# Performance work log

Hardware: AMD Instinct MI355X
Metric: run time of the kernel (lower is better)

Reference implementation:

```python
import jax, jax.numpy as jnp
import numpy as np


def conv(x, w, b=None, stride=1, pad=0):
    out = jax.lax.conv_general_dilated(x, w, (stride, stride), [(pad, pad), (pad, pad)],
                                       dimension_numbers=('NCHW', 'OIHW', 'NCHW'))
    if b is not None:
        out = out + b[None, :, None, None]
    return out


def fsm(x, att_w, conv_w):
    # FeatureSelectionModule: global-avg-pool -> 1x1 conv -> sigmoid gate, residual, 1x1 proj
    gap = jnp.mean(x, axis=(2, 3), keepdims=True)
    atten = jax.nn.sigmoid(conv(gap, att_w))
    return conv(x + x * atten, conv_w)


def mdcn(x, offset, mask, weight, bias, pad=1, G=8):
    # Modulated deformable conv v2: stride 1, dilation 1, conv groups 1, G deformable groups.
    N, C, H, W = x.shape
    Co, Ci, kh, kw = weight.shape
    K = kh * kw
    Cg = C // G
    off = offset.reshape(N, G, 2, K, H, W)          # per-group (y, x) offsets per kernel tap
    msk = mask.reshape(N, G, 1, K, H, W)
    ky, kx = jnp.meshgrid(jnp.arange(kh), jnp.arange(kw), indexing='ij')
    py = (jnp.arange(H, dtype=x.dtype)[None, None, None, :, None] - pad) + ky.reshape(1, 1, K, 1, 1) + off[:, :, 0]
    px = (jnp.arange(W, dtype=x.dtype)[None, None, None, None, :] - pad) + kx.reshape(1, 1, K, 1, 1) + off[:, :, 1]
    y0 = jnp.floor(py)
    x0 = jnp.floor(px)
    wy1 = py - y0
    wy0 = 1.0 - wy1
    wx1 = px - x0
    wx0 = 1.0 - wx1
    xg = x.reshape(N, G, Cg, H * W)

    def gather(iy, ix):
        valid = (iy >= 0) & (iy <= H - 1) & (ix >= 0) & (ix <= W - 1)
        idx = (jnp.clip(iy, 0, H - 1) * W + jnp.clip(ix, 0, W - 1)).astype(jnp.int32)
        v = jnp.take_along_axis(xg, idx.reshape(N, G, 1, K * H * W), axis=3)
        return v.reshape(N, G, Cg, K, H, W) * valid[:, :, None].astype(x.dtype)

    val = ((wy0 * wx0)[:, :, None] * gather(y0, x0)
         + (wy0 * wx1)[:, :, None] * gather(y0, x0 + 1)
         + (wy1 * wx0)[:, :, None] * gather(y0 + 1, x0)
         + (wy1 * wx1)[:, :, None] * gather(y0 + 1, x0 + 1))
    val = val * msk                                   # [N,G,Cg,K,H,W]
    out = jnp.einsum('ngckhw,ogck->nohw', val, weight.reshape(Co, G, Cg, K))
    return out + bias[None, :, None, None]


def align(feat_l, feat_s, att_w, fsm_w, off_w, om_w, om_b, dcn_w, dcn_b):
    # FeatureAlign_V2
    N, Cs, H, W = feat_s.shape[0], feat_s.shape[1], feat_l.shape[2], feat_l.shape[3]
    feat_up = jax.image.resize(feat_s, (N, Cs, H, W), 'bilinear')  # align_corners=False
    feat_arm = fsm(feat_l, att_w, fsm_w)
    off_feat = conv(jnp.concatenate([feat_arm, feat_up * 2.0], axis=1), off_w)
    om = conv(off_feat, om_w, om_b, pad=1)            # conv_offset_mask: 3*G*K channels
    o1, o2, mk = jnp.split(om, 3, axis=1)
    offset = jnp.concatenate([o1, o2], axis=1)
    mask = jax.nn.sigmoid(mk)
    feat_align = jax.nn.relu(mdcn(feat_up, offset, mask, dcn_w, dcn_b))
    return feat_align + feat_arm


def setup_inputs() -> dict:
    key = jax.random.key(0)
    ks = iter(jax.random.split(key, 64))

    def w(shape):
        fan_in = shape[1] * shape[2] * shape[3]
        return jax.random.normal(next(ks), shape, jnp.float32) / np.float32(np.sqrt(fan_in))

    def b(n):
        return jnp.zeros((n,), jnp.float32)

    d = {}
    d['c2'] = jax.random.normal(next(ks), (1, 256, 128, 128), jnp.float32)
    d['c3'] = jax.random.normal(next(ks), (1, 512, 64, 64), jnp.float32)
    d['c4'] = jax.random.normal(next(ks), (1, 1024, 32, 32), jnp.float32)
    d['c5'] = jax.random.normal(next(ks), (1, 2048, 16, 16), jnp.float32)
    OC = 256
    OM = 8 * 3 * 9  # deformable_groups * (2 offsets + 1 mask) * k*k = 216
    for tag, in_nc in (('16', 1024), ('8', 512), ('4', 256)):
        d['att_w' + tag] = w((in_nc, in_nc, 1, 1))
        d['fsm_w' + tag] = w((OC, in_nc, 1, 1))
        d['off_w' + tag] = w((OC, 2 * OC, 1, 1))
        d['om_w' + tag] = w((OM, OC, 3, 3))
        d['om_b' + tag] = b(OM)
        d['dcn_w' + tag] = w((OC, OC, 3, 3))
        d['dcn_b' + tag] = b(OC)
        d['out_w' + tag] = w((OC, OC, 3, 3))
        d['out_b' + tag] = b(OC)
    d['lat_w'] = w((OC, 2048, 1, 1))
    d['lat_b'] = b(OC)
    return d


def reference(c2, c3, c4, c5,
              att_w16, fsm_w16, off_w16, om_w16, om_b16, dcn_w16, dcn_b16, out_w16, out_b16,
              att_w8, fsm_w8, off_w8, om_w8, om_b8, dcn_w8, dcn_b8, out_w8, out_b8,
              att_w4, fsm_w4, off_w4, om_w4, om_b4, dcn_w4, dcn_b4, out_w4, out_b4,
              lat_w, lat_b):
    # top-down pass, coarsest first (matches FAN.forward with reversed inputs)
    p5 = conv(c5, lat_w, lat_b)
    f16 = align(c4, p5, att_w16, fsm_w16, off_w16, om_w16, om_b16, dcn_w16, dcn_b16)
    p4 = conv(f16, out_w16, out_b16, pad=1)
    f8 = align(c3, f16, att_w8, fsm_w8, off_w8, om_w8, om_b8, dcn_w8, dcn_b8)
    p3 = conv(f8, out_w8, out_b8, pad=1)
    f4 = align(c2, f8, att_w4, fsm_w4, off_w4, om_w4, om_b4, dcn_w4, dcn_b4)
    p2 = conv(f4, out_w4, out_b4, pad=1)
    return (p2, p3, p4, p5)
```

## Files before the change

kernel.cpp:

```cpp
#include <hip/hip_runtime.h>
#include <hip/hip_bf16.h>

typedef __hip_bfloat16 bf16;
typedef __attribute__((ext_vector_type(8))) short bf16x8;
typedef __attribute__((ext_vector_type(4))) float floatx4;

__device__ __forceinline__ float b2f(bf16 v) { return __bfloat162float(v); }
__device__ __forceinline__ bf16 f2b(float v) { return __float2bfloat16(v); }
__device__ __forceinline__ float us2f(unsigned short u) {
  union { unsigned int i; float f; } v; v.i = ((unsigned int)u) << 16; return v.f;
}
__device__ __forceinline__ unsigned short f2us(float f) {
  bf16 h = f2b(f); return *(unsigned short*)&h;
}

__global__ __launch_bounds__(256) void gap_kernel(const float* __restrict__ x,
                                                  float* __restrict__ gap,
                                                  int HW, float inv) {
  int c = blockIdx.x;
  const float* p = x + (size_t)c * HW;
  float s = 0.f;
  for (int i = threadIdx.x; i < HW; i += 256) s += p[i];
  __shared__ float red[256];
  red[threadIdx.x] = s;
  __syncthreads();
  for (int w = 128; w > 0; w >>= 1) {
    if (threadIdx.x < w) red[threadIdx.x] += red[threadIdx.x + w];
    __syncthreads();
  }
  if (threadIdx.x == 0) gap[c] = red[0] * inv;
}

__global__ __launch_bounds__(256) void atten_kernel(const float* __restrict__ w,
                                                    const float* __restrict__ gap,
                                                    float* __restrict__ scale, int Ci) {
  int wave = threadIdx.x >> 6, lane = threadIdx.x & 63;
  int o = blockIdx.x * 4 + wave;
  const float4* wr = (const float4*)(w + (size_t)o * Ci);
  const float4* g4 = (const float4*)gap;
  int n4 = Ci >> 2;
  float s = 0.f;
  for (int i = lane; i < n4; i += 64) {
    float4 a = wr[i], b = g4[i];
    s += a.x * b.x + a.y * b.y + a.z * b.z + a.w * b.w;
  }
#pragma unroll
  for (int off = 32; off > 0; off >>= 1) s += __shfl_down(s, off);
  if (lane == 0) scale[o] = 1.f + 1.f / (1.f + expf(-s));
}

__global__ __launch_bounds__(256) void upsample2x_nhwc_kernel(
    const bf16* __restrict__ src, bf16* __restrict__ dst, int Hs, int Ws) {
  int p = blockIdx.x;
  int c = threadIdx.x;
  int W = Ws * 2;
  int y = p / W, x = p - y * W;
  float fy = y * 0.5f - 0.25f;
  float fx = x * 0.5f - 0.25f;
  int y0 = (int)floorf(fy), x0 = (int)floorf(fx);
  float wy1 = fy - (float)y0, wx1 = fx - (float)x0;
  int y0c = min(max(y0, 0), Hs - 1);
  int y1c = min(max(y0 + 1, 0), Hs - 1);
  int x0c = min(max(x0, 0), Ws - 1);
  int x1c = min(max(x0 + 1, 0), Ws - 1);
  float v00 = b2f(src[(size_t)(y0c * Ws + x0c) * 256 + c]);
  float v01 = b2f(src[(size_t)(y0c * Ws + x1c) * 256 + c]);
  float v10 = b2f(src[(size_t)(y1c * Ws + x0c) * 256 + c]);
  float v11 = b2f(src[(size_t)(y1c * Ws + x1c) * 256 + c]);
  float v = (1.f - wy1) * ((1.f - wx1) * v00 + wx1 * v01)
          + wy1 * ((1.f - wx1) * v10 + wx1 * v11);
  dst[(size_t)p * 256 + c] = f2b(v);
}

__global__ __launch_bounds__(256) void packw1_kernel(const float* __restrict__ w,
                                                     bf16* __restrict__ BP, int K) {
  int idx = blockIdx.x * 256 + threadIdx.x;
  int j = idx & 7;
  int o = (idx >> 3) & 255;
  int kc8 = idx >> 11;
  int k = kc8 * 8 + j;
  BP[idx] = f2b(w[(size_t)o * K + k]);
}

__global__ __launch_bounds__(256) void packwd_kernel(const float* __restrict__ w,
                                                     bf16* __restrict__ BP) {
  int idx = blockIdx.x * 256 + threadIdx.x;
  int j = idx & 7;
  int o = (idx >> 3) & 255;
  int k8 = idx >> 11;
  int k = k8 * 8 + j;
  int tap = k >> 8;
  int ci = k & 255;
  BP[idx] = f2b(w[((size_t)o * 256 + ci) * 9 + tap]);
}

__global__ __launch_bounds__(256) void packw3_kernel(const float* __restrict__ w,
                                                     bf16* __restrict__ BP,
                                                     int Ci, int Co) {
  int idx = blockIdx.x * 256 + threadIdx.x;
  int total = Ci * 9 * 256;
  if (idx >= total) return;
  int j = idx & 7;
  int t1 = idx >> 3;
  int o = t1 & 255;
  int t2 = t1 >> 8;
  int q = t2 & 3;
  int t3 = t2 >> 2;
  int tap = t3 % 9;
  int c = t3 / 9;
  int ci = c * 32 + q * 8 + j;
  float v = (o < Co) ? w[((size_t)o * Ci + ci) * 9 + tap] : 0.f;
  BP[idx] = f2b(v);
}

template <bool NCHW1, typename TA1>
__global__ __launch_bounds__(256) void conv1x1_mfma_kernel(
    const TA1* __restrict__ A1, const float* __restrict__ scaleA,
    const bf16* __restrict__ A2, float scaleB,
    int Ci1, int Ci2, int HW,
    const bf16* __restrict__ BP, const float* __restrict__ bias,
    float* __restrict__ out1, bf16* __restrict__ out2, int ns2) {
  __shared__ __align__(16) bf16 sA[1024];
  int p0 = blockIdx.x * 32;
  int tid = threadIdx.x;
  int pix = tid & 31, sub = tid >> 5;
  int pix2 = tid >> 3, sub8 = tid & 7;
  int lane = tid & 63, wave = tid >> 6;
  int pg = wave & 1, cg = wave >> 1;
  int q = lane >> 4, n = lane & 15;

  floatx4 acc[4];
#pragma unroll
  for (int nt = 0; nt < 4; ++nt) acc[nt] = (floatx4)0.f;

  int nch = (Ci1 + Ci2) >> 5;
  for (int kc = 0; kc < nch; ++kc) {
    int ci0 = kc << 5;
    if (NCHW1 && ci0 < Ci1) {
#pragma unroll
      for (int it = 0; it < 4; ++it) {
        int cil = it * 8 + sub;
        float x = (float)A1[(size_t)(ci0 + cil) * HW + p0 + pix];
        if (scaleA) x *= scaleA[ci0 + cil];
        sA[((cil >> 3) * 32 + pix) * 8 + (cil & 7)] = f2b(x);
      }
    } else {
      const bf16* src; int cb; bool scl;
      if (!NCHW1 && ci0 < Ci1) {
        src = (const bf16*)(const void*)A1; cb = ci0; scl = false;
      } else {
        src = A2; cb = ci0 - Ci1; scl = true;
      }
      ushort4 raw = *(const ushort4*)&src[(size_t)(p0 + pix2) * 256 + cb + sub8 * 4];
      if (scl) {
        raw.x = f2us(us2f(raw.x) * scaleB);
        raw.y = f2us(us2f(raw.y) * scaleB);
        raw.z = f2us(us2f(raw.z) * scaleB);
        raw.w = f2us(us2f(raw.w) * scaleB);
      }
      *(ushort4*)&sA[((sub8 >> 1) * 32 + pix2) * 8 + (sub8 & 1) * 4] = raw;
    }
    __syncthreads();
    bf16x8 a = *(const bf16x8*)&sA[(q * 32 + pg * 16 + n) * 8];
    const bf16* bp = BP + ((size_t)(kc * 4 + q) * 256 + blockIdx.y * 128 + cg * 64) * 8;
#pragma unroll
    for (int nt = 0; nt < 4; ++nt) {
      bf16x8 b = *(const bf16x8*)&bp[(nt * 16 + n) * 8];
      acc[nt] = __builtin_amdgcn_mfma_f32_16x16x32_bf16(a, b, acc[nt], 0, 0, 0);
    }
    __syncthreads();
  }

  int pbase = p0 + pg * 16 + q * 4;
#pragma unroll
  for (int nt = 0; nt < 4; ++nt) {
    int o = blockIdx.y * 128 + cg * 64 + nt * 16 + n;
    float bv = bias ? bias[o] : 0.f;
#pragma unroll
    for (int r = 0; r < 4; ++r) {
      float v = acc[nt][r] + bv;
      if (out1) out1[(size_t)o * HW + pbase + r] = v;
      if (out2) out2[(size_t)(pbase + r) * ns2 + o] = f2b(v);
    }
  }
}

__global__ __launch_bounds__(256) void conv1x1_part_kernel(
    const float* __restrict__ A1, int HW,
    const bf16* __restrict__ BP, float* __restrict__ PART) {
  __shared__ __align__(16) bf16 sA[1024];
  int p0 = blockIdx.x * 32;
  int tid = threadIdx.x;
  int pix = tid & 31, sub = tid >> 5;
  int lane = tid & 63, wave = tid >> 6;
  int pg = wave & 1, cg = wave >> 1;
  int q = lane >> 4, n = lane & 15;

  floatx4 acc[4];
#pragma unroll
  for (int nt = 0; nt < 4; ++nt) acc[nt] = (floatx4)0.f;

  int kc0 = blockIdx.z * 8;
  for (int kcl = 0; kcl < 8; ++kcl) {
    int kc = kc0 + kcl;
    int ci0 = kc << 5;
#pragma unroll
    for (int it = 0; it < 4; ++it) {
      int cil = it * 8 + sub;
      sA[((cil >> 3) * 32 + pix) * 8 + (cil & 7)] =
          f2b(A1[(size_t)(ci0 + cil) * HW + p0 + pix]);
    }
    __syncthreads();
    bf16x8 a = *(const bf16x8*)&sA[(q * 32 + pg * 16 + n) * 8];
    const bf16* bp = BP + ((size_t)(kc * 4 + q) * 256 + blockIdx.y * 128 + cg * 64) * 8;
#pragma unroll
    for (int nt = 0; nt < 4; ++nt) {
      bf16x8 b = *(const bf16x8*)&bp[(nt * 16 + n) * 8];
      acc[nt] = __builtin_amdgcn_mfma_f32_16x16x32_bf16(a, b, acc[nt], 0, 0, 0);
    }
    __syncthreads();
  }

  int pbase = p0 + pg * 16 + q * 4;
#pragma unroll
  for (int nt = 0; nt < 4; ++nt) {
    int o = blockIdx.y * 128 + cg * 64 + nt * 16 + n;
#pragma unroll
    for (int r = 0; r < 4; ++r)
      PART[((size_t)blockIdx.z * 256 + o) * HW + pbase + r] = acc[nt][r];
  }
}

__global__ __launch_bounds__(256) void reduce_p5_kernel(
    const float* __restrict__ PART, const float* __restrict__ bias,
    float* __restrict__ out1, bf16* __restrict__ out2, int HW, int KS) {
  int o = blockIdx.x;
  int p = threadIdx.x;
  float s = bias[o];
  for (int z = 0; z < KS; ++z) s += PART[((size_t)z * 256 + o) * HW + p];
  out1[(size_t)o * HW + p] = s;
  out2[(size_t)p * 256 + o] = f2b(s);
}

template <int S>
__global__ __launch_bounds__(256) void conv3x3v2_kernel(
    const bf16* __restrict__ in, const bf16* __restrict__ BP,
    const float* __restrict__ bias,
    int H, int W, int Co,
    float* __restrict__ out1, bf16* __restrict__ out2, int ns2) {
  constexpr int P = 32 * S + 2;
  constexpr int TASKS = 3 * P * 8;
  constexpr int ITS = (TASKS + 255) / 256;
  __shared__ __align__(16) bf16 sA[2][4 * 3 * P * 8];
  int HW = H * W;
  int segs = W / (32 * S);
  int y = blockIdx.x / segs;
  int x0 = (blockIdx.x - y * segs) * (32 * S);
  int tid = threadIdx.x;
  int lane = tid & 63, wave = tid >> 6;
  int pg = wave & 1, cg = wave >> 1;
  int q = lane >> 4, n = lane & 15;

  int dstIdx[ITS], srcOff[ITS];
  bool act[ITS], val[ITS];
#pragma unroll
  for (int it = 0; it < ITS; ++it) {
    int tt = it * 256 + tid;
    act[it] = (tt < TASKS);
    int sub8 = tt & 7;
    int rp = tt >> 3;
    int row = rp / P;
    int pxl = rp - row * P;
    int yy = y + row - 1;
    int xg = x0 + pxl - 1;
    bool v = act[it] && ((unsigned)yy < (unsigned)H) && ((unsigned)xg < (unsigned)W);
    val[it] = v;
    srcOff[it] = v ? ((yy * W + xg) * 256 + sub8 * 4) : 0;
    dstIdx[it] = (((sub8 >> 1) * 3 + row) * P + pxl) * 8 + (sub8 & 1) * 4;
  }

  ushort4 pv[ITS];
  auto load_regs = [&](int kc) {
    int cb = kc << 5;
#pragma unroll
    for (int it = 0; it < ITS; ++it) {
      ushort4 z = {0, 0, 0, 0};
      pv[it] = val[it] ? *(const ushort4*)&in[(size_t)srcOff[it] + cb] : z;
    }
  };
  auto store_lds = [&](int buf) {
#pragma unroll
    for (int it = 0; it < ITS; ++it)
      if (act[it]) *(ushort4*)&sA[buf][dstIdx[it]] = pv[it];
  };

  floatx4 acc[S][4];
#pragma unroll
  for (int s = 0; s < S; ++s)
#pragma unroll
    for (int nt = 0; nt < 4; ++nt) acc[s][nt] = (floatx4)0.f;

  load_regs(0);
  store_lds(0);
  __syncthreads();
  load_regs(1);

  for (int kc = 0; kc < 8; ++kc) {
    const bf16* sv = &sA[kc & 1][0];
    const bf16* bpc = BP + (size_t)kc * 73728;
#pragma unroll
    for (int tap = 0; tap < 9; ++tap) {
      int ty = tap / 3, tx = tap % 3;
      bf16x8 a[S];
#pragma unroll
      for (int s = 0; s < S; ++s)
        a[s] = *(const bf16x8*)&sv[((q * 3 + ty) * P + tx + s * 32 + pg * 16 + n) * 8];
      const bf16* bp = bpc + ((size_t)(tap * 4 + q) * 256 + blockIdx.y * 128 + cg * 64) * 8;
#pragma unroll
      for (int nt = 0; nt < 4; ++nt) {
        bf16x8 b = *(const bf16x8*)&bp[(nt * 16 + n) * 8];
#pragma unroll
        for (int s = 0; s < S; ++s)
          acc[s][nt] = __builtin_amdgcn_mfma_f32_16x16x32_bf16(a[s], b, acc[s][nt], 0, 0, 0);
      }
    }
    if (kc < 7) {
      store_lds((kc + 1) & 1);
      __syncthreads();
      if (kc < 6) load_regs(kc + 2);
    }
  }

#pragma unroll
  for (int s = 0; s < S; ++s) {
    int pbase = y * W + x0 + s * 32 + pg * 16 + q * 4;
#pragma unroll
    for (int nt = 0; nt < 4; ++nt) {
      int o = blockIdx.y * 128 + cg * 64 + nt * 16 + n;
      if (o < Co) {
        float bv = bias ? bias[o] : 0.f;
#pragma unroll
        for (int r = 0; r < 4; ++r) {
          float v = acc[s][nt][r] + bv;
          if (out1) out1[(size_t)o * HW + pbase + r] = v;
          if (out2) out2[(size_t)(pbase + r) * ns2 + o] = f2b(v);
        }
      }
    }
  }
}

__global__ __launch_bounds__(512, 4) void mdcn_mfma_kernel(
    const bf16* __restrict__ UPn, const bf16* __restrict__ OM,
    const bf16* __restrict__ BP, const float* __restrict__ dcn_b,
    const bf16* __restrict__ ARM, bf16* __restrict__ F,
    int H, int W, int wshift) {
  __shared__ __align__(16) bf16 sval[2][32 * 272];
  __shared__ float4 mw[2304];
  __shared__ int mi[2304];
  int pb = blockIdx.x * 32;
  int tid = threadIdx.x;

  for (int t2 = tid; t2 < 2304; t2 += 512) {
    int px_ = t2 & 31, g = (t2 >> 5) & 7, tap = t2 >> 8;
    int ky = tap / 3, kx = tap - ky * 3;
    int p = pb + px_;
    int y = p >> wshift, x = p & (W - 1);
    const bf16* omp = OM + (size_t)p * 216;
    float dy = b2f(omp[g * 18 + tap]);
    float dx = b2f(omp[g * 18 + 9 + tap]);
    float mm = 1.f / (1.f + expf(-b2f(omp[144 + g * 9 + tap])));
    float fpy = (float)(y - 1 + ky) + dy;
    float fpx = (float)(x - 1 + kx) + dx;
    fpy = fminf(fmaxf(fpy, -1.0e4f), 1.0e4f);
    fpx = fminf(fmaxf(fpx, -1.0e4f), 1.0e4f);
    float fy0 = floorf(fpy), fx0 = floorf(fpx);
    float wy1 = fpy - fy0, wx1 = fpx - fx0;
    float wy0 = 1.f - wy1, wx0 = 1.f - wx1;
    int iy0 = (int)fy0, ix0 = (int)fx0;
    bool vy0 = (unsigned)iy0 < (unsigned)H;
    bool vy1 = (unsigned)(iy0 + 1) < (unsigned)H;
    bool vx0 = (unsigned)ix0 < (unsigned)W;
    bool vx1 = (unsigned)(ix0 + 1) < (unsigned)W;
    float w00 = (vy0 && vx0) ? mm * wy0 * wx0 : 0.f;
    float w01 = (vy0 && vx1) ? mm * wy0 * wx1 : 0.f;
    float w10 = (vy1 && vx0) ? mm * wy1 * wx0 : 0.f;
    float w11 = (vy1 && vx1) ? mm * wy1 * wx1 : 0.f;
    int iy0c = min(max(iy0, 0), H - 1);
    int iy1c = min(max(iy0 + 1, 0), H - 1);
    int ix0c = min(max(ix0, 0), W - 1);
    int ix1c = min(max(ix0 + 1, 0), W - 1);
    mw[t2] = make_float4(w00, w01, w10, w11);
    mi[t2] = (iy0c * W + ix0c) | ((ix1c - ix0c) << 20) | ((iy1c - iy0c) << 21);
  }
  __syncthreads();

  int l4 = tid & 7;
  int px = (tid >> 3) & 31;
  int gh = tid >> 8;
  int lane = tid & 63, wave = tid >> 6;
  int q = lane >> 4, n = lane & 15;
  int rowb = l4 >> 1;
  int woff = px * 8 + (l4 & 1) * 4;

  floatx4 acc[2][2];
#pragma unroll
  for (int m = 0; m < 2; ++m)
#pragma unroll
    for (int nt = 0; nt < 2; ++nt) acc[m][nt] = (floatx4)0.f;

  auto gather = [&](int t) {
    bf16* sv = &sval[t & 1][0];
    int base = t * 256 + px + gh * 128;
#pragma unroll
    for (int gg = 0; gg < 4; ++gg) {
      int g = gh * 4 + gg;
      float4 wv = mw[base + gg * 32];
      int mv = mi[base + gg * 32];
      int idx = mv & 0x3FFFF;
      int dxs = (mv >> 20) & 1;
      int dyW = ((mv >> 21) & 1) * W;
      const bf16* up = UPn + (size_t)idx * 256 + g * 32 + l4 * 4;
      ushort4 u00 = *(const ushort4*)(up);
      ushort4 u01 = *(const ushort4*)(up + dxs * 256);
      ushort4 u10 = *(const ushort4*)(up + dyW * 256);
      ushort4 u11 = *(const ushort4*)(up + (dyW + dxs) * 256);
      ushort4 o4;
      o4.x = f2us(wv.x * us2f(u00.x) + wv.y * us2f(u01.x)
                + wv.z * us2f(u10.x) + wv.w * us2f(u11.x));
      o4.y = f2us(wv.x * us2f(u00.y) + wv.y * us2f(u01.y)
                + wv.z * us2f(u10.y) + wv.w * us2f(u11.y));
      o4.z = f2us(wv.x * us2f(u00.z) + wv.y * us2f(u01.z)
                + wv.z * us2f(u10.z) + wv.w * us2f(u11.z));
      o4.w = f2us(wv.x * us2f(u00.w) + wv.y * us2f(u01.w)
                + wv.z * us2f(u10.w) + wv.w * us2f(u11.w));
      *(ushort4*)&sv[(g * 4 + rowb) * 272 + woff] = o4;
    }
  };

  gather(0);
  for (int t = 0; t < 9; ++t) {
    __syncthreads();
    if (t < 8) gather(t + 1);
    const bf16* sv = &sval[t & 1][0];
    const bf16* bpt = BP + ((size_t)(t * 32) * 256 + wave * 32) * 8;
#pragma unroll
    for (int kc = 0; kc < 8; ++kc) {
      int R = kc * 4 + q;
      bf16x8 a0 = *(const bf16x8*)&sv[R * 272 + n * 8];
      bf16x8 a1 = *(const bf16x8*)&sv[R * 272 + (16 + n) * 8];
      const bf16* bp = bpt + (size_t)R * 2048;
      bf16x8 b0 = *(const bf16x8*)&bp[n * 8];
      bf16x8 b1 = *(const bf16x8*)&bp[(16 + n) * 8];
      acc[0][0] = __builtin_amdgcn_mfma_f32_16x16x32_bf16(a0, b0, acc[0][0], 0, 0, 0);
      acc[0][1] = __builtin_amdgcn_mfma_f32_16x16x32_bf16(a0, b1, acc[0][1], 0, 0, 0);
      acc[1][0] = __builtin_amdgcn_mfma_f32_16x16x32_bf16(a1, b0, acc[1][0], 0, 0, 0);
      acc[1][1] = __builtin_amdgcn_mfma_f32_16x16x32_bf16(a1, b1, acc[1][1], 0, 0, 0);
    }
  }

#pragma unroll
  for (int m = 0; m < 2; ++m) {
#pragma unroll
    for (int nt = 0; nt < 2; ++nt) {
      int o = wave * 32 + nt * 16 + n;
      float bv = dcn_b[o];
#pragma unroll
      for (int r = 0; r < 4; ++r) {
        int p = pb + m * 16 + q * 4 + r;
        float v = fmaxf(acc[m][nt][r] + bv, 0.f) + b2f(ARM[(size_t)p * 256 + o]);
        F[(size_t)p * 256 + o] = f2b(v);
      }
    }
  }
}

extern "C" void kernel_launch(void* const* d_in, const int* in_sizes, int n_in,
                              void* d_out, int out_size, void* d_ws, size_t ws_size,
                              hipStream_t stream) {
  const float* c2 = (const float*)d_in[0];
  const float* c3 = (const float*)d_in[1];
  const float* c4 = (const float*)d_in[2];
  const float* c5 = (const float*)d_in[3];
  const float* lat_w = (const float*)d_in[31];
  const float* lat_b = (const float*)d_in[32];
  float* out = (float*)d_out;
  (void)ws_size; (void)in_sizes; (void)n_in; (void)out_size;

  const size_t p2_off = 0;
  const size_t p3_off = 4194304;
  const size_t p4_off = p3_off + 1048576;
  const size_t p5_off = p4_off + 262144;

  char* ws = (char*)d_ws;
  bf16* UPn = (bf16*)(ws);
  bf16* ARM = (bf16*)(ws + 8388608);
  bf16* FB  = (bf16*)(ws + 16777216);
  bf16* P5N = (bf16*)(ws + 25165824);
  bf16* BPB = (bf16*)(ws + 25296896);
  float* GAP = (float*)(ws + 26476544);
  float* SC  = (float*)(ws + 26484736);
  bf16* OM = (bf16*)(out + p2_off);
  float* PART = (float*)ws;

  packw1_kernel<<<2048, 256, 0, stream>>>(lat_w, BPB, 2048);
  conv1x1_part_kernel<<<dim3(8, 2, 8), 256, 0, stream>>>(c5, 256, BPB, PART);
  reduce_p5_kernel<<<256, 256, 0, stream>>>(PART, lat_b, out + p5_off, P5N, 256, 8);

  struct Lv {
    const float* featl; int Ci; int H; int W; int wshift;
    float* pdst; int wbase;
  };
  Lv levels[3] = {
      {c4, 1024, 32, 32, 5, out + p4_off, 4},
      {c3, 512, 64, 64, 6, out + p3_off, 13},
      {c2, 256, 128, 128, 7, out + p2_off, 22},
  };

  for (int li = 0; li < 3; ++li) {
    const Lv& L = levels[li];
    const float* att_w = (const float*)d_in[L.wbase + 0];
    const float* fsm_w = (const float*)d_in[L.wbase + 1];
    const float* off_w = (const float*)d_in[L.wbase + 2];
    const float* om_w  = (const float*)d_in[L.wbase + 3];
    const float* om_b  = (const float*)d_in[L.wbase + 4];
    const float* dcn_w = (const float*)d_in[L.wbase + 5];
    const float* dcn_b = (const float*)d_in[L.wbase + 6];
    const float* out_w = (const float*)d_in[L.wbase + 7];
    const float* out_b = (const float*)d_in[L.wbase + 8];
    int HW = L.H * L.W;

    upsample2x_nhwc_kernel<<<HW, 256, 0, stream>>>(
        (li == 0) ? P5N : FB, UPn, L.H / 2, L.W / 2);
    gap_kernel<<<L.Ci, 256, 0, stream>>>(L.featl, GAP, HW, 1.f / (float)HW);
    atten_kernel<<<L.Ci / 4, 256, 0, stream>>>(att_w, GAP, SC, L.Ci);
    packw1_kernel<<<L.Ci, 256, 0, stream>>>(fsm_w, BPB, L.Ci);
    conv1x1_mfma_kernel<true, float><<<dim3(HW / 32, 2), 256, 0, stream>>>(
        L.featl, SC, nullptr, 0.f, L.Ci, 0, HW, BPB, nullptr,
        nullptr, ARM, 256);
    packw1_kernel<<<512, 256, 0, stream>>>(off_w, BPB, 512);
    conv1x1_mfma_kernel<false, bf16><<<dim3(HW / 32, 2), 256, 0, stream>>>(
        ARM, nullptr, UPn, 2.f, 256, 256, HW, BPB, nullptr,
        nullptr, FB, 256);
    packw3_kernel<<<2304, 256, 0, stream>>>(om_w, BPB, 256, 216);
    if (li == 2)
      conv3x3v2_kernel<2><<<dim3(HW / 64, 2), 256, 0, stream>>>(
          FB, BPB, om_b, L.H, L.W, 216, nullptr, OM, 216);
    else
      conv3x3v2_kernel<1><<<dim3(HW / 32, 2), 256, 0, stream>>>(
          FB, BPB, om_b, L.H, L.W, 216, nullptr, OM, 216);
    packwd_kernel<<<2304, 256, 0, stream>>>(dcn_w, BPB);
    mdcn_mfma_kernel<<<HW / 32, 512, 0, stream>>>(
        UPn, OM, BPB, dcn_b, ARM, FB, L.H, L.W, L.wshift);
    packw3_kernel<<<2304, 256, 0, stream>>>(out_w, BPB, 256, 256);
    if (li == 2)
      conv3x3v2_kernel<2><<<dim3(HW / 64, 2), 256, 0, stream>>>(
          FB, BPB, out_b, L.H, L.W, 256, L.pdst, nullptr, 256);
    else
      conv3x3v2_kernel<1><<<dim3(HW / 32, 2), 256, 0, stream>>>(
          FB, BPB, out_b, L.H, L.W, 256, L.pdst, nullptr, 256);
  }
}
```

Before: 723.7 us.

## Fuse per-level weight packing into one launch and overlap MDCN gathers with MFMA

Per level, the five separate weight-packing launches are merged into one pack_level_kernel that writes into distinct buffers, so per-launch overhead drops and packs no longer serialize between convolutions. Some packed buffers are placed in unused parts of the output region. In the deformable conv kernel, the gather is split into a global-load phase issued before the MFMA loop and a blend/store phase after it, so memory latency hides behind matrix math. This costs 64 extra ushort registers per thread, which may lower occupancy, and relies on output scratch space not being overwritten before use.

```diff
diff --git a/kernel.cpp b/kernel.cpp
--- a/kernel.cpp
+++ b/kernel.cpp
@@ -82,24 +82,40 @@
   BP[idx] = f2b(w[(size_t)o * K + k]);
 }
 
-__global__ __launch_bounds__(256) void packwd_kernel(const float* __restrict__ w,
-                                                     bf16* __restrict__ BP) {
-  int idx = blockIdx.x * 256 + threadIdx.x;
-  int j = idx & 7;
-  int o = (idx >> 3) & 255;
-  int k8 = idx >> 11;
-  int k = k8 * 8 + j;
-  int tap = k >> 8;
-  int ci = k & 255;
-  BP[idx] = f2b(w[((size_t)o * 256 + ci) * 9 + tap]);
-}
-
-__global__ __launch_bounds__(256) void packw3_kernel(const float* __restrict__ w,
-                                                     bf16* __restrict__ BP,
-                                                     int Ci, int Co) {
-  int idx = blockIdx.x * 256 + threadIdx.x;
-  int total = Ci * 9 * 256;
-  if (idx >= total) return;
+__global__ __launch_bounds__(256) void pack_level_kernel(
+    const float* __restrict__ fsm_w, int Ci,
+    const float* __restrict__ off_w, const float* __restrict__ om_w,
+    const float* __restrict__ dcn_w, const float* __restrict__ out_w,
+    bf16* __restrict__ BPfsm, bf16* __restrict__ BPoff, bf16* __restrict__ BPom,
+    bf16* __restrict__ BPdcn, bf16* __restrict__ BPout) {
+  int b = blockIdx.x;
+  if (b < Ci) {
+    int idx = b * 256 + threadIdx.x;
+    int j = idx & 7, o = (idx >> 3) & 255, k = (idx >> 11) * 8 + j;
+    BPfsm[idx] = f2b(fsm_w[(size_t)o * Ci + k]);
+    return;
+  }
+  b -= Ci;
+  if (b < 512) {
+    int idx = b * 256 + threadIdx.x;
+    int j = idx & 7, o = (idx >> 3) & 255, k = (idx >> 11) * 8 + j;
+    BPoff[idx] = f2b(off_w[(size_t)o * 512 + k]);
+    return;
+  }
+  b -= 512;
+  const float* w;
+  bf16* BP;
+  int Co;
+  if (b < 2304) { w = om_w; BP = BPom; Co = 216; }
+  else if (b < 4608) {
+    int idx = (b - 2304) * 256 + threadIdx.x;
+    int j = idx & 7, o = (idx >> 3) & 255;
+    int k = (idx >> 11) * 8 + j;
+    int tap = k >> 8, ci = k & 255;
+    BPdcn[idx] = f2b(dcn_w[((size_t)o * 256 + ci) * 9 + tap]);
+    return;
+  } else { w = out_w; BP = BPout; Co = 256; b -= 2304; }
+  int idx = (b % 2304) * 256 + threadIdx.x;
   int j = idx & 7;
   int t1 = idx >> 3;
   int o = t1 & 255;
@@ -109,7 +125,7 @@
   int tap = t3 % 9;
   int c = t3 / 9;
   int ci = c * 32 + q * 8 + j;
-  float v = (o < Co) ? w[((size_t)o * Ci + ci) * 9 + tap] : 0.f;
+  float v = (o < Co) ? w[((size_t)o * 256 + ci) * 9 + tap] : 0.f;
   BP[idx] = f2b(v);
 }
 
@@ -409,22 +425,31 @@
 #pragma unroll
     for (int nt = 0; nt < 2; ++nt) acc[m][nt] = (floatx4)0.f;
 
-  auto gather = [&](int t) {
-    bf16* sv = &sval[t & 1][0];
+  ushort4 gl[4][4];
+  auto gatherLoad = [&](int t) {
     int base = t * 256 + px + gh * 128;
 #pragma unroll
     for (int gg = 0; gg < 4; ++gg) {
       int g = gh * 4 + gg;
-      float4 wv = mw[base + gg * 32];
       int mv = mi[base + gg * 32];
       int idx = mv & 0x3FFFF;
       int dxs = (mv >> 20) & 1;
       int dyW = ((mv >> 21) & 1) * W;
       const bf16* up = UPn + (size_t)idx * 256 + g * 32 + l4 * 4;
-      ushort4 u00 = *(const ushort4*)(up);
-      ushort4 u01 = *(const ushort4*)(up + dxs * 256);
-      ushort4 u10 = *(const ushort4*)(up + dyW * 256);
-      ushort4 u11 = *(const ushort4*)(up + (dyW + dxs) * 256);
+      gl[gg][0] = *(const ushort4*)(up);
+      gl[gg][1] = *(const ushort4*)(up + dxs * 256);
+      gl[gg][2] = *(const ushort4*)(up + dyW * 256);
+      gl[gg][3] = *(const ushort4*)(up + (dyW + dxs) * 256);
+    }
+  };
+  auto gatherStore = [&](int t) {
+    bf16* sv = &sval[t & 1][0];
+    int base = t * 256 + px + gh * 128;
+#pragma unroll
+    for (int gg = 0; gg < 4; ++gg) {
+      int g = gh * 4 + gg;
+      float4 wv = mw[base + gg * 32];
+      ushort4 u00 = gl[gg][0], u01 = gl[gg][1], u10 = gl[gg][2], u11 = gl[gg][3];
       ushort4 o4;
       o4.x = f2us(wv.x * us2f(u00.x) + wv.y * us2f(u01.x)
                 + wv.z * us2f(u10.x) + wv.w * us2f(u11.x));
@@ -438,10 +463,11 @@
     }
   };
 
-  gather(0);
+  gatherLoad(0);
+  gatherStore(0);
   for (int t = 0; t < 9; ++t) {
     __syncthreads();
-    if (t < 8) gather(t + 1);
+    if (t < 8) gatherLoad(t + 1);
     const bf16* sv = &sval[t & 1][0];
     const bf16* bpt = BP + ((size_t)(t * 32) * 256 + wave * 32) * 8;
 #pragma unroll
@@ -457,6 +483,7 @@
       acc[1][0] = __builtin_amdgcn_mfma_f32_16x16x32_bf16(a1, b0, acc[1][0], 0, 0, 0);
       acc[1][1] = __builtin_amdgcn_mfma_f32_16x16x32_bf16(a1, b1, acc[1][1], 0, 0, 0);
     }
+    if (t < 8) gatherStore(t + 1);
   }
 
 #pragma unroll
@@ -497,14 +524,18 @@
   bf16* ARM = (bf16*)(ws + 8388608);
   bf16* FB  = (bf16*)(ws + 16777216);
   bf16* P5N = (bf16*)(ws + 25165824);
-  bf16* BPB = (bf16*)(ws + 25296896);
-  float* GAP = (float*)(ws + 26476544);
-  float* SC  = (float*)(ws + 26484736);
+  bf16* BPout = (bf16*)(ws + 25296896);
+  bf16* BPfsm = (bf16*)(ws + 26476544);
+  bf16* BPoff = (bf16*)(ws + 27000832);
+  float* GAP = (float*)(ws + 27262976);
+  float* SC  = (float*)(ws + 27271168);
   bf16* OM = (bf16*)(out + p2_off);
+  bf16* BPom = (bf16*)((char*)(out + p2_off) + 10485760);
+  bf16* BPdcn = (bf16*)((char*)(out + p2_off) + 11665408);
   float* PART = (float*)ws;
 
-  packw1_kernel<<<2048, 256, 0, stream>>>(lat_w, BPB, 2048);
-  conv1x1_part_kernel<<<dim3(8, 2, 8), 256, 0, stream>>>(c5, 256, BPB, PART);
+  packw1_kernel<<<2048, 256, 0, stream>>>(lat_w, BPout, 2048);
+  conv1x1_part_kernel<<<dim3(8, 2, 8), 256, 0, stream>>>(c5, 256, BPout, PART);
   reduce_p5_kernel<<<256, 256, 0, stream>>>(PART, lat_b, out + p5_off, P5N, 256, 8);
 
   struct Lv {
@@ -530,34 +561,32 @@
     const float* out_b = (const float*)d_in[L.wbase + 8];
     int HW = L.H * L.W;
 
+    pack_level_kernel<<<L.Ci + 512 + 3 * 2304, 256, 0, stream>>>(
+        fsm_w, L.Ci, off_w, om_w, dcn_w, out_w,
+        BPfsm, BPoff, BPom, BPdcn, BPout);
     upsample2x_nhwc_kernel<<<HW, 256, 0, stream>>>(
         (li == 0) ? P5N : FB, UPn, L.H / 2, L.W / 2);
     gap_kernel<<<L.Ci, 256, 0, stream>>>(L.featl, GAP, HW, 1.f / (float)HW);
     atten_kernel<<<L.Ci / 4, 256, 0, stream>>>(att_w, GAP, SC, L.Ci);
-    packw1_kernel<<<L.Ci, 256, 0, stream>>>(fsm_w, BPB, L.Ci);
     conv1x1_mfma_kernel<true, float><<<dim3(HW / 32, 2), 256, 0, stream>>>(
-        L.featl, SC, nullptr, 0.f, L.Ci, 0, HW, BPB, nullptr,
+        L.featl, SC, nullptr, 0.f, L.Ci, 0, HW, BPfsm, nullptr,
         nullptr, ARM, 256);
-    packw1_kernel<<<512, 256, 0, stream>>>(off_w, BPB, 512);
     conv1x1_mfma_kernel<false, bf16><<<dim3(HW / 32, 2), 256, 0, stream>>>(
-        ARM, nullptr, UPn, 2.f, 256, 256, HW, BPB, nullptr,
+        ARM, nullptr, UPn, 2.f, 256, 256, HW, BPoff, nullptr,
         nullptr, FB, 256);
-    packw3_kernel<<<2304, 256, 0, stream>>>(om_w, BPB, 256, 216);
     if (li == 2)
       conv3x3v2_kernel<2><<<dim3(HW / 64, 2), 256, 0, stream>>>(
-          FB, BPB, om_b, L.H, L.W, 216, nullptr, OM, 216);
+          FB, BPom, om_b, L.H, L.W, 216, nullptr, OM, 216);
     else
       conv3x3v2_kernel<1><<<dim3(HW / 32, 2), 256, 0, stream>>>(
-          FB, BPB, om_b, L.H, L.W, 216, nullptr, OM, 216);
-    packwd_kernel<<<2304, 256, 0, stream>>>(dcn_w, BPB);
+          FB, BPom, om_b, L.H, L.W, 216, nullptr, OM, 216);
     mdcn_mfma_kernel<<<HW / 32, 512, 0, stream>>>(
-        UPn, OM, BPB, dcn_b, ARM, FB, L.H, L.W, L.wshift);
-    packw3_kernel<<<2304, 256, 0, stream>>>(out_w, BPB, 256, 256);
+        UPn, OM, BPdcn, dcn_b, ARM, FB, L.H, L.W, L.wshift);
     if (li == 2)
       conv3x3v2_kernel<2><<<dim3(HW / 64, 2), 256, 0, stream>>>(
-          FB, BPB, out_b, L.H, L.W, 256, L.pdst, nullptr, 256);
+          FB, BPout, out_b, L.H, L.W, 256, L.pdst, nullptr, 256);
     else
       conv3x3v2_kernel<1><<<dim3(HW / 32, 2), 256, 0, stream>>>(
-          FB, BPB, out_b, L.H, L.W, 256, L.pdst, nullptr, 256);
-  }
-}
+          FB, BPout, out_b, L.H, L.W, 256, L.pdst, nullptr, 256);
+  }
+}
```

Result: faster. 696.4 us (-3.8%).
